# Kernel optimization log

Hardware: AMD Instinct MI355X
Metric: run time of the kernel (lower is better)

The kernel has to match this reference:

```python
import jax, jax.numpy as jnp
import numpy as np

N = 200000
K = 16
D = 32
IN_SIZE = K * (K - 1) // 2  # 120
HID = 128


def setup_inputs() -> dict:
    key = jax.random.key(0)
    ks = jax.random.split(key, 12)
    E = N * K
    x = jax.random.normal(ks[0], (N, D), dtype=jnp.float32)
    edge_attr = jax.random.normal(ks[1], (E, D), dtype=jnp.float32)
    # kNN-style edge_index: source node i owns edges [i*K, (i+1)*K)
    src = jnp.repeat(jnp.arange(N, dtype=jnp.int64), K)
    dst = jax.random.randint(ks[2], (E,), 0, N, dtype=jnp.int64)
    edge_index = jnp.stack([src, dst], axis=0)
    s = 0.1
    W1 = jax.random.normal(ks[3], (IN_SIZE, HID), dtype=jnp.float32) * s
    b1 = jnp.zeros((HID,), dtype=jnp.float32)
    W2 = jax.random.normal(ks[4], (HID, HID), dtype=jnp.float32) * s
    b2 = jnp.zeros((HID,), dtype=jnp.float32)
    W3 = jax.random.normal(ks[5], (HID, HID), dtype=jnp.float32) * s
    b3 = jnp.zeros((HID,), dtype=jnp.float32)
    W4 = jax.random.normal(ks[6], (HID, 1), dtype=jnp.float32) * s
    b4 = jnp.zeros((1,), dtype=jnp.float32)
    return {"x": x, "edge_index": edge_index, "edge_attr": edge_attr, "k": K,
            "W1": W1, "b1": b1, "W2": W2, "b2": b2, "W3": W3, "b3": b3,
            "W4": W4, "b4": b4}


def calc_pair_angles(edge_attr, k):
    # edge_attr: [N*k, d] per-edge neighbor vectors, grouped k per node
    E, d = edge_attr.shape
    n = E // k
    v = edge_attr.reshape(n, k, d)
    vn = v / (jnp.linalg.norm(v, axis=-1, keepdims=True) + 1e-12)
    cos = jnp.einsum('nkd,nmd->nkm', vn, vn)  # [n, k, k]
    cos = jnp.clip(cos, -1.0 + 1e-7, 1.0 - 1e-7)
    ang = jnp.arccos(cos)
    iu, ju = jnp.triu_indices(k, 1)
    return ang[:, iu, ju]  # [n, k*(k-1)/2]


def reference(x, edge_index, edge_attr, k, W1, b1, W2, b2, W3, b3, W4, b4):
    # message() returns edge_attr; aggregate() computes pairwise neighbor angles
    feats = calc_pair_angles(edge_attr, k)  # [N, 120]
    h = jnp.tanh(feats @ W1 + b1)
    h = jnp.tanh(h @ W2 + b2)
    h = jnp.tanh(h @ W3 + b3)
    out = jax.nn.sigmoid(h @ W4 + b4)  # [N, 1]
    return out[:, 0]  # squeeze, [N]
```

## Files before the change

kernel.cpp:

```cpp
#include <hip/hip_runtime.h>
#include <hip/hip_bf16.h>
#include <math.h>


#define NTHREADS 256
#define CHUNK    16
#define ASTRIDE  136
#define PBLOCKS  512

typedef _Float16 f16;
typedef f16  f16x8 __attribute__((ext_vector_type(8)));
typedef f16  f16x4 __attribute__((ext_vector_type(4)));
typedef float f32x4 __attribute__((ext_vector_type(4)));

#define MFMA16(a, b, c) __builtin_amdgcn_mfma_f32_16x16x32_f16(a, b, c, 0, 0, 0)

__device__ __forceinline__ float fast_tanh(float x) {
    float e = __expf(2.0f * x);
    return 1.0f - 2.0f * __builtin_amdgcn_rcpf(e + 1.0f);
}

__device__ __forceinline__ float fast_acos(float x) {
    float ax = fabsf(x);
    float p = fmaf(-0.0187293f, ax, 0.0742610f);
    p = fmaf(p, ax, -0.2121144f);
    p = fmaf(p, ax, 1.5707288f);
    float r = sqrtf(1.0f - ax) * p;
    return (x >= 0.0f) ? r : (3.14159265358979f - r);
}

__device__ __forceinline__ void load_lds16(const float* g, float* l) {
    __builtin_amdgcn_global_load_lds(
        (__attribute__((address_space(1))) void*)(g),
        (__attribute__((address_space(3))) void*)(l), 16, 0, 0);
}

__global__ void prep_weights(const float* __restrict__ W1,
                             const float* __restrict__ W2,
                             const float* __restrict__ W3,
                             f16* __restrict__ wt)
{
    int tid = blockIdx.x * 256 + threadIdx.x;
    if (tid >= 3 * 128 * 128) return;
    int layer = tid >> 14;
    int rem   = tid & 16383;
    int j     = rem >> 7;
    int i     = rem & 127;
    const float* W = (layer == 0) ? W1 : ((layer == 1) ? W2 : W3);
    int in_l = (layer == 0) ? 120 : 128;
    float v = (i < in_l) ? W[i * 128 + j] : 0.0f;
    wt[tid] = (f16)v;
}

__global__ __launch_bounds__(NTHREADS, 2)
void gnn_pipe(const float* __restrict__ edge_attr,
              const f16*   __restrict__ wt,
              const float* __restrict__ b1, const float* __restrict__ b2,
              const float* __restrict__ b3,
              const float* __restrict__ W4, const float* __restrict__ b4,
              float* __restrict__ out, int n_nodes, int nchunks)
{
    __shared__ __attribute__((aligned(16))) float stg[2][8192];
    __shared__ __attribute__((aligned(16))) f16   actA[16 * ASTRIDE];
    __shared__ __attribute__((aligned(16))) f16   actB[16 * ASTRIDE];
    __shared__ __attribute__((aligned(16))) float diag[4][4][16];
    __shared__ __attribute__((aligned(16))) float pbuf[16][4];

    const int t  = threadIdx.x;
    const int w  = t >> 6;
    const int l  = t & 63;
    const int lr = l & 15;
    const int lg = l >> 4;

    if (t < 128) actA[(t >> 3) * ASTRIDE + 120 + (t & 7)] = (f16)0.f;

    #define LW(L, jj, kt) (*(const f16x8*)(wt + (L) * 16384 + ((w * 2 + (jj)) * 16 + lr) * 128 + (kt) * 32 + lg * 8))
    const f16x8 W000 = LW(0,0,0), W001 = LW(0,0,1), W002 = LW(0,0,2), W003 = LW(0,0,3);
    const f16x8 W010 = LW(0,1,0), W011 = LW(0,1,1), W012 = LW(0,1,2), W013 = LW(0,1,3);
    const f16x8 W100 = LW(1,0,0), W101 = LW(1,0,1), W102 = LW(1,0,2), W103 = LW(1,0,3);
    const f16x8 W110 = LW(1,1,0), W111 = LW(1,1,1), W112 = LW(1,1,2), W113 = LW(1,1,3);
    const f16x8 W200 = LW(2,0,0), W201 = LW(2,0,1), W202 = LW(2,0,2), W203 = LW(2,0,3);
    const f16x8 W210 = LW(2,1,0), W211 = LW(2,1,1), W212 = LW(2,1,2), W213 = LW(2,1,3);
    #undef LW
    const f32x4 bva0 = *(const f32x4*)(b1 + (w * 2 + 0) * 16 + lg * 4);
    const f32x4 bva1 = *(const f32x4*)(b1 + (w * 2 + 1) * 16 + lg * 4);
    const f32x4 bvb0 = *(const f32x4*)(b2 + (w * 2 + 0) * 16 + lg * 4);
    const f32x4 bvb1 = *(const f32x4*)(b2 + (w * 2 + 1) * 16 + lg * 4);
    const f32x4 bvc0 = *(const f32x4*)(b3 + (w * 2 + 0) * 16 + lg * 4);
    const f32x4 bvc1 = *(const f32x4*)(b3 + (w * 2 + 1) * 16 + lg * 4);
    const f32x4 w4v0 = *(const f32x4*)(W4 + w * 32 + lg * 4);
    const f32x4 w4v1 = *(const f32x4*)(W4 + w * 32 + 16 + lg * 4);
    const float bb4  = b4[0];

    const int swsrc = (l * 16) ^ ((l >> 3) << 4);

    #define STAGE(ch_, b_)                                                       \
        {                                                                        \
            const long n0_ = (long)(ch_) * CHUNK + w * 4;                        \
            _Pragma("unroll")                                                    \
            for (int i_ = 0; i_ < 8; ++i_) {                                     \
                long nd_ = n0_ + (i_ >> 1);                                      \
                if (nd_ >= n_nodes) nd_ = n_nodes - 1;                           \
                const float* gs_ = (const float*)((const char*)edge_attr         \
                                   + nd_ * 2048 + (i_ & 1) * 1024 + swsrc);      \
                load_lds16(gs_, &stg[b_][w * 2048 + i_ * 256]);                  \
            }                                                                    \
        }

    #define LBAR()                                                               \
        {                                                                        \
            asm volatile("s_waitcnt lgkmcnt(0)" ::: "memory");                   \
            __builtin_amdgcn_s_barrier();                                        \
            __builtin_amdgcn_sched_barrier(0);                                   \
        }

    #define LAYER(SRC, DST, Wa0, Wa1, Wa2, Wa3, Wb0, Wb1, Wb2, Wb3, BV0, BV1)   \
        {                                                                        \
            const f16* sr_ = SRC + lr * ASTRIDE + lg * 8;                        \
            f16x8 s0_ = *(const f16x8*)(sr_);                                    \
            f16x8 s1_ = *(const f16x8*)(sr_ + 32);                               \
            f16x8 s2_ = *(const f16x8*)(sr_ + 64);                               \
            f16x8 s3_ = *(const f16x8*)(sr_ + 96);                               \
            f32x4 a0_ = {0.f, 0.f, 0.f, 0.f}, a1_ = a0_;                         \
            a0_ = MFMA16(Wa0, s0_, a0_); a1_ = MFMA16(Wb0, s0_, a1_);            \
            a0_ = MFMA16(Wa1, s1_, a0_); a1_ = MFMA16(Wb1, s1_, a1_);            \
            a0_ = MFMA16(Wa2, s2_, a0_); a1_ = MFMA16(Wb2, s2_, a1_);            \
            a0_ = MFMA16(Wa3, s3_, a0_); a1_ = MFMA16(Wb3, s3_, a1_);            \
            f16x4 o0_, o1_;                                                      \
            _Pragma("unroll")                                                    \
            for (int r_ = 0; r_ < 4; ++r_) {                                     \
                o0_[r_] = (f16)fast_tanh(a0_[r_] + BV0[r_]);                     \
                o1_[r_] = (f16)fast_tanh(a1_[r_] + BV1[r_]);                     \
            }                                                                    \
            *(f16x4*)(DST + lr * ASTRIDE + (w * 2 + 0) * 16 + lg * 4) = o0_;     \
            *(f16x4*)(DST + lr * ASTRIDE + (w * 2 + 1) * 16 + lg * 4) = o1_;     \
        }

    #define LAYER3(SRC)                                                          \
        {                                                                        \
            const f16* sr_ = (SRC) + lr * ASTRIDE + lg * 8;                      \
            f16x8 s0_ = *(const f16x8*)(sr_);                                    \
            f16x8 s1_ = *(const f16x8*)(sr_ + 32);                               \
            f16x8 s2_ = *(const f16x8*)(sr_ + 64);                               \
            f16x8 s3_ = *(const f16x8*)(sr_ + 96);                               \
            f32x4 a0_ = {0.f, 0.f, 0.f, 0.f}, a1_ = a0_;                         \
            a0_ = MFMA16(W200, s0_, a0_); a1_ = MFMA16(W210, s0_, a1_);          \
            a0_ = MFMA16(W201, s1_, a0_); a1_ = MFMA16(W211, s1_, a1_);          \
            a0_ = MFMA16(W202, s2_, a0_); a1_ = MFMA16(W212, s2_, a1_);          \
            a0_ = MFMA16(W203, s3_, a0_); a1_ = MFMA16(W213, s3_, a1_);          \
            float p_ = 0.f;                                                      \
            _Pragma("unroll")                                                    \
            for (int r_ = 0; r_ < 4; ++r_) {                                     \
                p_ = fmaf(fast_tanh(a0_[r_] + bvc0[r_]), w4v0[r_], p_);          \
                p_ = fmaf(fast_tanh(a1_[r_] + bvc1[r_]), w4v1[r_], p_);          \
            }                                                                    \
            p_ += __shfl_xor(p_, 16);                                            \
            p_ += __shfl_xor(p_, 32);                                            \
            if (l < 16) pbuf[lr][w] = p_;                                        \
        }

    #define FINALSUM(ch_)                                                        \
        {                                                                        \
            if (t < 16) {                                                        \
                f32x4 pv_ = *(const f32x4*)&pbuf[t][0];                          \
                float s_ = (pv_[0] + pv_[1]) + (pv_[2] + pv_[3]);                \
                const long gn_ = (long)(ch_) * CHUNK + t;                        \
                if (gn_ < n_nodes)                                               \
                    out[gn_] = __builtin_amdgcn_rcpf(1.0f + __expf(-(s_ + bb4)));\
            }                                                                    \
        }

    long ch = blockIdx.x;
    STAGE(ch, 0);
    asm volatile("s_waitcnt vmcnt(0)" ::: "memory");
    __builtin_amdgcn_sched_barrier(0);

    int it = 0;
    for (; ch < nchunks; ch += PBLOCKS, ++it) {
        const int b = it & 1;
        if (it) {
            asm volatile("s_waitcnt vmcnt(1)" ::: "memory");
            __builtin_amdgcn_sched_barrier(0);
        }

        const char* ws_ = (const char*)&stg[b][w * 2048];
        const int abase = lr * 128 + lg * 32;
        const int akey  = (lr & 7) << 4;
        f16x8 f0, f1, f2, f3;
        #define FRAG(fc, m_)                                                     \
            {                                                                    \
                float4 va = *(const float4*)(ws_ + (m_) * 2048 + (abase ^ akey));        \
                float4 vb = *(const float4*)(ws_ + (m_) * 2048 + ((abase + 16) ^ akey)); \
                fc[0]=(f16)va.x; fc[1]=(f16)va.y; fc[2]=(f16)va.z; fc[3]=(f16)va.w;      \
                fc[4]=(f16)vb.x; fc[5]=(f16)vb.y; fc[6]=(f16)vb.z; fc[7]=(f16)vb.w;      \
            }
        FRAG(f0, 0) FRAG(f1, 1) FRAG(f2, 2) FRAG(f3, 3)
        #undef FRAG

        const long nxt = ch + PBLOCKS;
        if (nxt < nchunks) STAGE(nxt, b ^ 1);

        f32x4 g0, g1, g2, g3;
        {
            f32x4 z = {0.f, 0.f, 0.f, 0.f};
            g0 = MFMA16(f0, f0, z); g1 = MFMA16(f1, f1, z);
            g2 = MFMA16(f2, f2, z); g3 = MFMA16(f3, f3, z);
        }
        if (lg == (lr >> 2)) {
            const int r = lr & 3;
            diag[w][0][lr] = __builtin_amdgcn_rsqf(g0[r] + 1e-24f);
            diag[w][1][lr] = __builtin_amdgcn_rsqf(g1[r] + 1e-24f);
            diag[w][2][lr] = __builtin_amdgcn_rsqf(g2[r] + 1e-24f);
            diag[w][3][lr] = __builtin_amdgcn_rsqf(g3[r] + 1e-24f);
        }
        asm volatile("s_waitcnt lgkmcnt(0)" ::: "memory");
        __builtin_amdgcn_sched_barrier(0);

        #define FIN(gc, c)                                                       \
            {                                                                    \
                const float rc = diag[w][c][lr];                                 \
                const f32x4 rr = *(const f32x4*)&diag[w][c][lg * 4];             \
                const int m_ = w * 4 + (c);                                      \
                const int col = lr;                                              \
                _Pragma("unroll")                                                \
                for (int r2 = 0; r2 < 4; ++r2) {                                 \
                    const int row = lg * 4 + r2;                                 \
                    float cv = gc[r2] * rr[r2] * rc;                             \
                    cv = fminf(fmaxf(cv, -1.0f + 1e-7f), 1.0f - 1e-7f);          \
                    float ang = fast_acos(cv);                                   \
                    if (row < col) {                                             \
                        const int p = 15*row - ((row*(row-1))>>1) + (col-row-1); \
                        actA[m_ * ASTRIDE + p] = (f16)ang;                       \
                    }                                                            \
                }                                                                \
            }
        FIN(g0, 0) FIN(g1, 1) FIN(g2, 2) FIN(g3, 3)
        #undef FIN

        LBAR();

        LAYER(actA, actB, W000, W001, W002, W003, W010, W011, W012, W013, bva0, bva1);
        LBAR();
        LAYER(actB, actA, W100, W101, W102, W103, W110, W111, W112, W113, bvb0, bvb1);
        LBAR();
        LAYER3(actA);
        LBAR();

        FINALSUM(ch);
    }
    #undef STAGE
    #undef LBAR
    #undef LAYER
    #undef LAYER3
    #undef FINALSUM
}

extern "C" void kernel_launch(void* const* d_in, const int* in_sizes, int n_in,
                              void* d_out, int out_size, void* d_ws, size_t ws_size,
                              hipStream_t stream) {
    const float* edge_attr = (const float*)d_in[2];
    const float* W1 = (const float*)d_in[4];
    const float* b1 = (const float*)d_in[5];
    const float* W2 = (const float*)d_in[6];
    const float* b2 = (const float*)d_in[7];
    const float* W3 = (const float*)d_in[8];
    const float* b3 = (const float*)d_in[9];
    const float* W4 = (const float*)d_in[10];
    const float* b4 = (const float*)d_in[11];
    float* out = (float*)d_out;
    f16* wt = (f16*)d_ws;

    const int n_nodes = in_sizes[2] / 512;
    const int nchunks = (n_nodes + CHUNK - 1) / CHUNK;
    const int blocks  = PBLOCKS < nchunks ? PBLOCKS : nchunks;

    prep_weights<<<(3 * 128 * 128 + 255) / 256, 256, 0, stream>>>(W1, W2, W3, wt);

    gnn_pipe<<<blocks, NTHREADS, 0, stream>>>(
        edge_attr, wt, b1, b2, b3, W4, b4, out, n_nodes, nchunks);
}
```

Before: 123.3 us.

## Single-buffer staging and move biases to LDS to fit three blocks per CU

Drops the double-buffered edge_attr staging area down to one buffer. The next chunk's async load is now issued only after the current fragments have been read out of LDS. Biases and W4 move from registers into a shared constant buffer, and launch bounds and the persistent grid go from 2 to 3 blocks per CU. The intent is to raise occupancy by cutting LDS and register use. In exchange, the prefetch can only overlap the compute that follows the fragment reads, there are extra LDS reads per layer, and an lgkmcnt wait is added.

Result: faster. 116.1 us (-5.9%).

```diff
diff --git a/kernel.cpp b/kernel.cpp
--- a/kernel.cpp
+++ b/kernel.cpp
@@ -6,7 +6,7 @@
 #define NTHREADS 256
 #define CHUNK    16
 #define ASTRIDE  136
-#define PBLOCKS  512
+#define PBLOCKS  768
 
 typedef _Float16 f16;
 typedef f16  f16x8 __attribute__((ext_vector_type(8)));
@@ -52,7 +52,7 @@
     wt[tid] = (f16)v;
 }
 
-__global__ __launch_bounds__(NTHREADS, 2)
+__global__ __launch_bounds__(NTHREADS, 3)
 void gnn_pipe(const float* __restrict__ edge_attr,
               const f16*   __restrict__ wt,
               const float* __restrict__ b1, const float* __restrict__ b2,
@@ -60,11 +60,12 @@
               const float* __restrict__ W4, const float* __restrict__ b4,
               float* __restrict__ out, int n_nodes, int nchunks)
 {
-    __shared__ __attribute__((aligned(16))) float stg[2][8192];
+    __shared__ __attribute__((aligned(16))) float stg[8192];
     __shared__ __attribute__((aligned(16))) f16   actA[16 * ASTRIDE];
     __shared__ __attribute__((aligned(16))) f16   actB[16 * ASTRIDE];
     __shared__ __attribute__((aligned(16))) float diag[4][4][16];
     __shared__ __attribute__((aligned(16))) float pbuf[16][4];
+    __shared__ __attribute__((aligned(16))) float cbuf[512];
 
     const int t  = threadIdx.x;
     const int w  = t >> 6;
@@ -72,7 +73,14 @@
     const int lr = l & 15;
     const int lg = l >> 4;
 
-    if (t < 128) actA[(t >> 3) * ASTRIDE + 120 + (t & 7)] = (f16)0.f;
+    if (t < 128) {
+        cbuf[t]       = b1[t];
+        cbuf[128 + t] = b2[t];
+        cbuf[256 + t] = b3[t];
+        cbuf[384 + t] = W4[t];
+        actA[(t >> 3) * ASTRIDE + 120 + (t & 7)] = (f16)0.f;
+    }
+    const float bb4 = b4[0];
 
     #define LW(L, jj, kt) (*(const f16x8*)(wt + (L) * 16384 + ((w * 2 + (jj)) * 16 + lr) * 128 + (kt) * 32 + lg * 8))
     const f16x8 W000 = LW(0,0,0), W001 = LW(0,0,1), W002 = LW(0,0,2), W003 = LW(0,0,3);
@@ -82,19 +90,10 @@
     const f16x8 W200 = LW(2,0,0), W201 = LW(2,0,1), W202 = LW(2,0,2), W203 = LW(2,0,3);
     const f16x8 W210 = LW(2,1,0), W211 = LW(2,1,1), W212 = LW(2,1,2), W213 = LW(2,1,3);
     #undef LW
-    const f32x4 bva0 = *(const f32x4*)(b1 + (w * 2 + 0) * 16 + lg * 4);
-    const f32x4 bva1 = *(const f32x4*)(b1 + (w * 2 + 1) * 16 + lg * 4);
-    const f32x4 bvb0 = *(const f32x4*)(b2 + (w * 2 + 0) * 16 + lg * 4);
-    const f32x4 bvb1 = *(const f32x4*)(b2 + (w * 2 + 1) * 16 + lg * 4);
-    const f32x4 bvc0 = *(const f32x4*)(b3 + (w * 2 + 0) * 16 + lg * 4);
-    const f32x4 bvc1 = *(const f32x4*)(b3 + (w * 2 + 1) * 16 + lg * 4);
-    const f32x4 w4v0 = *(const f32x4*)(W4 + w * 32 + lg * 4);
-    const f32x4 w4v1 = *(const f32x4*)(W4 + w * 32 + 16 + lg * 4);
-    const float bb4  = b4[0];
 
     const int swsrc = (l * 16) ^ ((l >> 3) << 4);
 
-    #define STAGE(ch_, b_)                                                       \
+    #define STAGE(ch_)                                                           \
         {                                                                        \
             const long n0_ = (long)(ch_) * CHUNK + w * 4;                        \
             _Pragma("unroll")                                                    \
@@ -103,7 +102,7 @@
                 if (nd_ >= n_nodes) nd_ = n_nodes - 1;                           \
                 const float* gs_ = (const float*)((const char*)edge_attr         \
                                    + nd_ * 2048 + (i_ & 1) * 1024 + swsrc);      \
-                load_lds16(gs_, &stg[b_][w * 2048 + i_ * 256]);                  \
+                load_lds16(gs_, &stg[w * 2048 + i_ * 256]);                      \
             }                                                                    \
         }
 
@@ -114,8 +113,10 @@
             __builtin_amdgcn_sched_barrier(0);                                   \
         }
 
-    #define LAYER(SRC, DST, Wa0, Wa1, Wa2, Wa3, Wb0, Wb1, Wb2, Wb3, BV0, BV1)   \
-        {                                                                        \
+    #define LAYER(SRC, DST, Wa0, Wa1, Wa2, Wa3, Wb0, Wb1, Wb2, Wb3, BOFF)       \
+        {                                                                        \
+            const f32x4 BV0 = *(const f32x4*)&cbuf[(BOFF) + (w * 2 + 0) * 16 + lg * 4]; \
+            const f32x4 BV1 = *(const f32x4*)&cbuf[(BOFF) + (w * 2 + 1) * 16 + lg * 4]; \
             const f16* sr_ = SRC + lr * ASTRIDE + lg * 8;                        \
             f16x8 s0_ = *(const f16x8*)(sr_);                                    \
             f16x8 s1_ = *(const f16x8*)(sr_ + 32);                               \
@@ -138,6 +139,10 @@
 
     #define LAYER3(SRC)                                                          \
         {                                                                        \
+            const f32x4 bvc0 = *(const f32x4*)&cbuf[256 + (w * 2 + 0) * 16 + lg * 4]; \
+            const f32x4 bvc1 = *(const f32x4*)&cbuf[256 + (w * 2 + 1) * 16 + lg * 4]; \
+            const f32x4 w4v0 = *(const f32x4*)&cbuf[384 + w * 32 + lg * 4];      \
+            const f32x4 w4v1 = *(const f32x4*)&cbuf[384 + w * 32 + 16 + lg * 4]; \
             const f16* sr_ = (SRC) + lr * ASTRIDE + lg * 8;                      \
             f16x8 s0_ = *(const f16x8*)(sr_);                                    \
             f16x8 s1_ = *(const f16x8*)(sr_ + 32);                               \
@@ -161,29 +166,29 @@
 
     #define FINALSUM(ch_)                                                        \
         {                                                                        \
-            if (t < 16) {                                                        \
-                f32x4 pv_ = *(const f32x4*)&pbuf[t][0];                          \
+            if (l < 4) {                                                         \
+                const int nd_ = w * 4 + l;                                       \
+                f32x4 pv_ = *(const f32x4*)&pbuf[nd_][0];                        \
                 float s_ = (pv_[0] + pv_[1]) + (pv_[2] + pv_[3]);                \
-                const long gn_ = (long)(ch_) * CHUNK + t;                        \
+                const long gn_ = (long)(ch_) * CHUNK + nd_;                      \
                 if (gn_ < n_nodes)                                               \
                     out[gn_] = __builtin_amdgcn_rcpf(1.0f + __expf(-(s_ + bb4)));\
             }                                                                    \
         }
 
     long ch = blockIdx.x;
-    STAGE(ch, 0);
+    STAGE(ch);
     asm volatile("s_waitcnt vmcnt(0)" ::: "memory");
     __builtin_amdgcn_sched_barrier(0);
 
     int it = 0;
     for (; ch < nchunks; ch += PBLOCKS, ++it) {
-        const int b = it & 1;
         if (it) {
             asm volatile("s_waitcnt vmcnt(1)" ::: "memory");
             __builtin_amdgcn_sched_barrier(0);
         }
 
-        const char* ws_ = (const char*)&stg[b][w * 2048];
+        const char* ws_ = (const char*)&stg[w * 2048];
         const int abase = lr * 128 + lg * 32;
         const int akey  = (lr & 7) << 4;
         f16x8 f0, f1, f2, f3;
@@ -197,8 +202,11 @@
         FRAG(f0, 0) FRAG(f1, 1) FRAG(f2, 2) FRAG(f3, 3)
         #undef FRAG
 
+        asm volatile("s_waitcnt lgkmcnt(0)" ::: "memory");
+        __builtin_amdgcn_sched_barrier(0);
+
         const long nxt = ch + PBLOCKS;
-        if (nxt < nchunks) STAGE(nxt, b ^ 1);
+        if (nxt < nchunks) STAGE(nxt);
 
         f32x4 g0, g1, g2, g3;
         {
@@ -239,9 +247,9 @@
 
         LBAR();
 
-        LAYER(actA, actB, W000, W001, W002, W003, W010, W011, W012, W013, bva0, bva1);
-        LBAR();
-        LAYER(actB, actA, W100, W101, W102, W103, W110, W111, W112, W113, bvb0, bvb1);
+        LAYER(actA, actB, W000, W001, W002, W003, W010, W011, W012, W013, 0);
+        LBAR();
+        LAYER(actB, actA, W100, W101, W102, W103, W110, W111, W112, W113, 128);
         LBAR();
         LAYER3(actA);
         LBAR();
```
